# Kernel optimization log

Hardware: AMD Instinct MI355X
Metric: run time of the kernel (lower is better)

The kernel has to match this reference:

```python
import math
import jax, jax.numpy as jnp
import numpy as np

N = 50000       # num_nodes
D = 128         # input feature dim
OUT = 128       # output_dim
H = 8           # num_heads
F = OUT // H    # out_feats per head (= self_attn hidden_dim)
E_RAND = 800000 # random edges per graph (+ N self loops)
ALPHA = 0.8
BETA = 0.5


def _edges(key):
    k1, k2 = jax.random.split(key)
    src = jax.random.randint(k1, (E_RAND,), 0, N, dtype=jnp.int32)
    dst = jax.random.randint(k2, (E_RAND,), 0, N, dtype=jnp.int32)
    loop = jnp.arange(N, dtype=jnp.int32)  # dgl.add_self_loop
    return jnp.concatenate([src, loop]), jnp.concatenate([dst, loop])


def setup_inputs() -> dict:
    key = jax.random.key(0)
    ks = jax.random.split(key, 32)
    inp = {"x": jax.random.normal(ks[0], (N, D), jnp.float32)}
    inp["src_s"], inp["dst_s"] = _edges(ks[1])
    inp["src_t"], inp["dst_t"] = _edges(ks[2])
    inp["src_p"], inp["dst_p"] = _edges(ks[3])
    i = 4
    for v in ("s", "t", "p"):
        inp[f"W_{v}"] = jax.random.normal(ks[i], (OUT, D), jnp.float32) * 0.05; i += 1
        inp[f"al_{v}"] = jax.random.normal(ks[i], (H, F), jnp.float32) * 0.1; i += 1
        inp[f"ar_{v}"] = jax.random.normal(ks[i], (H, F), jnp.float32) * 0.1; i += 1
        inp[f"b_{v}"] = jnp.zeros((OUT,), jnp.float32)
    inp["Wq"] = jax.random.normal(ks[i], (F, OUT), jnp.float32) * 0.05; i += 1
    inp["bq"] = jnp.zeros((F,), jnp.float32)
    inp["Wk"] = jax.random.normal(ks[i], (F, OUT), jnp.float32) * 0.05; i += 1
    inp["bk"] = jnp.zeros((F,), jnp.float32)
    inp["Wm"] = jax.random.normal(ks[i], (1, N * OUT), jnp.float32) * 0.001; i += 1
    inp["bm"] = jnp.zeros((1,), jnp.float32)
    return inp


def _gat(x, src, dst, W, al, ar, b):
    # DGL GATConv (eval mode, negative_slope=0.2, activation=relu)
    feat = (x @ W.T).reshape(N, H, F)                      # [N,H,F]
    el = jnp.einsum('nhf,hf->nh', feat, al)                # [N,H]
    er = jnp.einsum('nhf,hf->nh', feat, ar)
    e = jax.nn.leaky_relu(el[src] + er[dst], 0.2)          # [E,H]
    m = jax.ops.segment_max(e, dst, num_segments=N)        # per-dst softmax
    ex = jnp.exp(e - m[dst])
    s = jax.ops.segment_sum(ex, dst, num_segments=N)
    attn = ex / s[dst]                                     # [E,H]
    out = jax.ops.segment_sum(feat[src] * attn[:, :, None], dst, num_segments=N)
    return jax.nn.relu(out + b.reshape(1, H, F)).reshape(N, OUT)


def reference(x, src_s, dst_s, src_t, dst_t, src_p, dst_p,
              W_s, al_s, ar_s, b_s, W_t, al_t, ar_t, b_t,
              W_p, al_p, ar_p, b_p, Wq, bq, Wk, bk, Wm, bm):
    s = _gat(x, src_s, dst_s, W_s, al_s, ar_s, b_s)
    t = _gat(x, src_t, dst_t, W_t, al_t, ar_t, b_t)
    p = _gat(x, src_p, dst_p, W_p, al_p, ar_p, b_p)
    views = jnp.stack([s, t, p])                           # [3,N,OUT]
    # self_attn: one scalar attention weight per view
    Q = jnp.einsum('vne,he->vnh', views, Wq) + bq          # [3,N,F]
    K = jnp.einsum('vne,he->vnh', views, Wk) + bk
    logits = jnp.sum(Q.reshape(3, -1) * K.reshape(3, -1), -1) / math.sqrt(F * N)
    w = jax.nn.softmax(logits)                             # [3]
    fused = w[:, None, None] * views
    views2 = ALPHA * fused + (1.0 - ALPHA) * views         # [3,N,OUT]
    # mv_attn: sigmoid-gated sum of views
    omega = jax.nn.sigmoid(views2.reshape(3, -1) @ Wm.T + bm)[:, 0]  # [3]
    mv = jnp.einsum('v,vne->ne', omega, views2)            # [N,OUT]
    result = BETA * views2 + (1.0 - BETA) * mv[None]       # [3,N,OUT]
    return mv, result
```

## Files before the change

### kernel.cpp

```cpp
#include <hip/hip_runtime.h>


#define N_NODES 50000
#define DIM 128
#define OUTD 128
#define NH 8
#define NF 16
#define NE 850000
#define NOFF 50001
#define NBUCK 49
#define BCAP 20480
#define BIN_EPT 8
#define BIN_EPB 2048

typedef float f32x4 __attribute__((ext_vector_type(4)));
typedef float f32x2 __attribute__((ext_vector_type(2)));
typedef __bf16 bf16x8 __attribute__((ext_vector_type(8)));
typedef unsigned short u16x8 __attribute__((ext_vector_type(8)));

static __device__ __forceinline__ float bf2f_lo(unsigned int u) {
  return __uint_as_float(u << 16);
}
static __device__ __forceinline__ float bf2f_hi(unsigned int u) {
  return __uint_as_float(u & 0xffff0000u);
}
static __device__ __forceinline__ f32x2 up2(unsigned int u) {
  f32x2 r;
  r.x = __uint_as_float(u << 16);
  r.y = __uint_as_float(u & 0xffff0000u);
  return r;
}
static __device__ __forceinline__ unsigned short f2bf(float f) {
  unsigned int u = __float_as_uint(f);
  unsigned int r = (u + 0x7fffu + ((u >> 16) & 1u)) >> 16;
  return (unsigned short)r;
}

__global__ __launch_bounds__(256) void gemm_feat_kernel(
    const float* __restrict__ x, const float* __restrict__ Ws,
    const float* __restrict__ Wt, const float* __restrict__ Wp,
    unsigned short* __restrict__ feat) {
  __shared__ unsigned short xa[128 * 128];
  __shared__ unsigned short wb[128 * 128];
  const int t = threadIdx.x;
  const int n0 = blockIdx.x * 128;

  for (int i = 0; i < 16; ++i) {
    int flat = (i * 256 + t) * 4;
    int r = flat >> 7, c = flat & 127;
    float4 val = make_float4(0.f, 0.f, 0.f, 0.f);
    if (n0 + r < N_NODES) val = *(const float4*)(x + (size_t)(n0 + r) * DIM + c);
    int byteoff = (r * 256 + c * 2) ^ ((r & 7) << 4);
    unsigned short* p = (unsigned short*)((char*)xa + byteoff);
    p[0] = f2bf(val.x); p[1] = f2bf(val.y); p[2] = f2bf(val.z); p[3] = f2bf(val.w);
  }

  const int wave = t >> 6, lane = t & 63;
  const int wr = wave >> 1, wc = wave & 1;
  const int lrow = lane & 15;
  const int kgrp = lane >> 4;

  for (int v = 0; v < 3; ++v) {
    const float* W = (v == 0) ? Ws : ((v == 1) ? Wt : Wp);
    __syncthreads();
    for (int i = 0; i < 16; ++i) {
      int flat = (i * 256 + t) * 4;
      int r = flat >> 7, c = flat & 127;
      float4 val = *(const float4*)(W + r * DIM + c);
      int byteoff = (r * 256 + c * 2) ^ ((r & 7) << 4);
      unsigned short* p = (unsigned short*)((char*)wb + byteoff);
      p[0] = f2bf(val.x); p[1] = f2bf(val.y); p[2] = f2bf(val.z); p[3] = f2bf(val.w);
    }
    __syncthreads();

    f32x4 acc[4][4];
    for (int m = 0; m < 4; ++m)
      for (int n = 0; n < 4; ++n) acc[m][n] = (f32x4)0.f;

    for (int ks = 0; ks < 4; ++ks) {
      bf16x8 af[4], bfr[4];
      int kb2 = (ks * 32 + kgrp * 8) * 2;
      for (int m = 0; m < 4; ++m) {
        int r = wr * 64 + m * 16 + lrow;
        af[m] = *(const bf16x8*)((const char*)xa + ((r * 256 + kb2) ^ ((r & 7) << 4)));
      }
      for (int n = 0; n < 4; ++n) {
        int r = wc * 64 + n * 16 + lrow;
        bfr[n] = *(const bf16x8*)((const char*)wb + ((r * 256 + kb2) ^ ((r & 7) << 4)));
      }
      for (int m = 0; m < 4; ++m)
        for (int n = 0; n < 4; ++n)
          acc[m][n] = __builtin_amdgcn_mfma_f32_16x16x32_bf16(af[m], bfr[n], acc[m][n], 0, 0, 0);
    }

    unsigned short* fv = feat + (size_t)v * N_NODES * OUTD;
    for (int m = 0; m < 4; ++m)
      for (int n = 0; n < 4; ++n) {
        int col = wc * 64 + n * 16 + lrow;
        for (int r4 = 0; r4 < 4; ++r4) {
          int row = n0 + wr * 64 + m * 16 + kgrp * 4 + r4;
          if (row < N_NODES) fv[(size_t)row * OUTD + col] = f2bf(acc[m][n][r4]);
        }
      }
  }
}

__global__ __launch_bounds__(256) void elr_kernel(
    const unsigned short* __restrict__ feat,
    const float* __restrict__ al_s, const float* __restrict__ ar_s,
    const float* __restrict__ al_t, const float* __restrict__ ar_t,
    const float* __restrict__ al_p, const float* __restrict__ ar_p,
    float* __restrict__ el, float* __restrict__ er) {
  int idx = blockIdx.x * 256 + threadIdx.x;
  if (idx >= 3 * N_NODES * NH) return;
  int v = idx / (N_NODES * NH);
  int rem = idx - v * (N_NODES * NH);
  int n = rem >> 3, h = rem & 7;
  const float* al = (v == 0) ? al_s : ((v == 1) ? al_t : al_p);
  const float* ar = (v == 0) ? ar_s : ((v == 1) ? ar_t : ar_p);
  const unsigned short* fr = feat + (size_t)v * N_NODES * OUTD + (size_t)n * OUTD + h * NF;
  uint4 a = *(const uint4*)(fr);
  uint4 b = *(const uint4*)(fr + 8);
  float fv[16];
  fv[0] = bf2f_lo(a.x); fv[1] = bf2f_hi(a.x); fv[2] = bf2f_lo(a.y); fv[3] = bf2f_hi(a.y);
  fv[4] = bf2f_lo(a.z); fv[5] = bf2f_hi(a.z); fv[6] = bf2f_lo(a.w); fv[7] = bf2f_hi(a.w);
  fv[8] = bf2f_lo(b.x); fv[9] = bf2f_hi(b.x); fv[10] = bf2f_lo(b.y); fv[11] = bf2f_hi(b.y);
  fv[12] = bf2f_lo(b.z); fv[13] = bf2f_hi(b.z); fv[14] = bf2f_lo(b.w); fv[15] = bf2f_hi(b.w);
  float accl = 0.f, accr = 0.f;
#pragma unroll
  for (int f = 0; f < NF; ++f) {
    accl += fv[f] * al[h * NF + f];
    accr += fv[f] * ar[h * NF + f];
  }
  el[idx] = accl;
  er[idx] = accr;
}

__global__ __launch_bounds__(256) void bin_kernel(
    const int* __restrict__ src_s, const int* __restrict__ dst_s,
    const int* __restrict__ src_t, const int* __restrict__ dst_t,
    const int* __restrict__ src_p, const int* __restrict__ dst_p,
    int* __restrict__ gtail, unsigned int* __restrict__ gbin) {
  const int v = blockIdx.y;
  const int* S = (v == 0) ? src_s : ((v == 1) ? src_t : src_p);
  const int* D = (v == 0) ? dst_s : ((v == 1) ? dst_t : dst_p);
  __shared__ int lhist[4][64], lbase[4][64];
  const int t = threadIdx.x;
  const int wave = t >> 6;
  ((int*)lhist)[t] = 0;
  __syncthreads();
  const int e0 = blockIdx.x * BIN_EPB + t * BIN_EPT;
  unsigned int pk[BIN_EPT];
  int bk[BIN_EPT], rk[BIN_EPT];
#pragma unroll
  for (int i = 0; i < BIN_EPT; ++i) {
    int e = e0 + i;
    if (e < NE) {
      unsigned int s = (unsigned int)S[e], d = (unsigned int)D[e];
      pk[i] = (s << 16) | d;
      bk[i] = (int)(d >> 10);
      rk[i] = atomicAdd(&lhist[wave][bk[i]], 1);
    } else {
      bk[i] = -1;
    }
  }
  __syncthreads();
  if (t < 64) {
    int c0 = lhist[0][t], c1 = lhist[1][t], c2 = lhist[2][t], c3 = lhist[3][t];
    int tot = c0 + c1 + c2 + c3;
    int gb = (tot > 0) ? atomicAdd(&gtail[v * 64 + t], tot) : 0;
    lbase[0][t] = gb;
    lbase[1][t] = gb + c0;
    lbase[2][t] = gb + c0 + c1;
    lbase[3][t] = gb + c0 + c1 + c2;
  }
  __syncthreads();
#pragma unroll
  for (int i = 0; i < BIN_EPT; ++i) {
    if (bk[i] >= 0) {
      int pos = lbase[wave][bk[i]] + rk[i];
      if (pos < BCAP)
        gbin[((size_t)v * 64 + bk[i]) * BCAP + pos] = pk[i];
    }
  }
}

__global__ __launch_bounds__(1024) void bucket_sort_kernel(
    const int* __restrict__ gtail, const unsigned int* __restrict__ gbin,
    int* __restrict__ offs, int* __restrict__ esrc) {
  __shared__ int lcur[1024];
  __shared__ int wsum[16];
  __shared__ int sh_bbase;
  __shared__ unsigned int sorted[BCAP];
  __shared__ int lhist[1024];
  const int v = blockIdx.y;
  const int b = blockIdx.x;
  const int t = threadIdx.x;
  const int wave = t >> 6, lane = t & 63;

  int cnt = gtail[v * 64 + b];
  if (cnt > BCAP) cnt = BCAP;
  const unsigned int* eb = gbin + ((size_t)v * 64 + b) * BCAP;

  if (t < 64) {
    int valb = (t < b) ? gtail[v * 64 + t] : 0;
#pragma unroll
    for (int m = 1; m < 64; m <<= 1) valb += __shfl_xor(valb, m, 64);
    if (t == 0) sh_bbase = valb;
  }
  lhist[t] = 0;
  __syncthreads();

  for (int e = t; e < cnt; e += 1024)
    atomicAdd(&lhist[eb[e] & 1023u], 1);
  __syncthreads();

  int val = lhist[t];
  int incl = val;
#pragma unroll
  for (int st = 1; st < 64; st <<= 1) {
    int o = __shfl_up(incl, st, 64);
    if (lane >= st) incl += o;
  }
  if (lane == 63) wsum[wave] = incl;
  __syncthreads();
  if (t < 64) {
    int wv = (lane < 16) ? wsum[lane] : 0;
    int winc = wv;
#pragma unroll
    for (int st = 1; st < 16; st <<= 1) {
      int o = __shfl_up(winc, st, 64);
      if (lane >= st) winc += o;
    }
    if (lane < 16) wsum[lane] = winc - wv;
  }
  __syncthreads();
  const int base = wsum[wave] + incl - val;
  lcur[t] = base;

  const int bbase = sh_bbase;
  if (b == 0 && t == 0) offs[v * NOFF] = 0;
  {
    int n = b * 1024 + t;
    if (n < N_NODES) offs[v * NOFF + n + 1] = bbase + base + val;
  }
  __syncthreads();

  for (int e = t; e < cnt; e += 1024) {
    unsigned int pk = eb[e];
    int pos = atomicAdd(&lcur[pk & 1023u], 1);
    sorted[pos] = pk >> 16;
  }
  __syncthreads();

  int* ev = esrc + (size_t)v * NE + bbase;
  for (int e = t; e < cnt; e += 1024) ev[e] = (int)sorted[e];
}

__global__ __launch_bounds__(256) void gat_kernel(
    const int* __restrict__ offs, const int* __restrict__ esrc,
    const float* __restrict__ el, const float* __restrict__ er,
    const unsigned short* __restrict__ feat,
    const float* __restrict__ b_s, const float* __restrict__ b_t,
    const float* __restrict__ b_p, float* __restrict__ views) {
  const int v = blockIdx.y;
  const int n = blockIdx.x * 4 + (threadIdx.x >> 6);
  const int lane = threadIdx.x & 63;
  const int g = lane >> 4;
  const int q = lane & 15;
  const int h = q >> 1;
  const int* off_v = offs + v * NOFF;
  const int off0 = off_v[n];
  const int deg = off_v[n + 1] - off0;
  const int* es = esrc + (size_t)v * NE + off0;
  const float* el_v = el + (size_t)v * N_NODES * NH;
  const float er_h = er[((size_t)v * N_NODES + n) * NH + h];
  const unsigned short* featv = feat + (size_t)v * N_NODES * OUTD;

  f32x2 acc2[4];
#pragma unroll
  for (int j = 0; j < 4; ++j) acc2[j] = (f32x2)0.f;
  float sm = 0.f;

  int e0 = g, e1 = 4 + g;
  bool v0 = e0 < deg, v1 = e1 < deg;
  int s0 = es[v0 ? e0 : 0];
  int s1 = es[v1 ? e1 : 0];
  float l0 = el_v[s0 * NH + h];
  float l1 = el_v[s1 * NH + h];
  uint4 pk0 = *(const uint4*)(featv + (size_t)s0 * OUTD + q * 8);
  uint4 pk1 = *(const uint4*)(featv + (size_t)s1 * OUTD + q * 8);

  for (int base = 0; base < deg; base += 8) {
    bool cv0 = v0, cv1 = v1;
    float cl0 = l0, cl1 = l1;
    uint4 cp0 = pk0, cp1 = pk1;
    int nb = base + 8;
    if (nb < deg) {
      e0 = nb + g; e1 = nb + 4 + g;
      v0 = e0 < deg; v1 = e1 < deg;
      s0 = es[v0 ? e0 : 0];
      s1 = es[v1 ? e1 : 0];
      l0 = el_v[s0 * NH + h];
      l1 = el_v[s1 * NH + h];
      pk0 = *(const uint4*)(featv + (size_t)s0 * OUTD + q * 8);
      pk1 = *(const uint4*)(featv + (size_t)s1 * OUTD + q * 8);
    }
    float val0 = cl0 + er_h;
    float val1 = cl1 + er_h;
    val0 = fmaxf(val0, 0.2f * val0);
    val1 = fmaxf(val1, 0.2f * val1);
    float aw0 = cv0 ? __expf(val0) : 0.f;
    float aw1 = cv1 ? __expf(val1) : 0.f;
    sm += aw0 + aw1;
    acc2[0] += aw0 * up2(cp0.x) + aw1 * up2(cp1.x);
    acc2[1] += aw0 * up2(cp0.y) + aw1 * up2(cp1.y);
    acc2[2] += aw0 * up2(cp0.z) + aw1 * up2(cp1.z);
    acc2[3] += aw0 * up2(cp0.w) + aw1 * up2(cp1.w);
  }

#pragma unroll
  for (int m = 16; m < 64; m <<= 1) {
    sm += __shfl_xor(sm, m, 64);
#pragma unroll
    for (int j = 0; j < 4; ++j) {
      acc2[j].x += __shfl_xor(acc2[j].x, m, 64);
      acc2[j].y += __shfl_xor(acc2[j].y, m, 64);
    }
  }

  if (g == 0) {
    const float inv = 1.0f / sm;
    const float* bv = (v == 0) ? b_s : ((v == 1) ? b_t : b_p);
    float r[8];
#pragma unroll
    for (int j = 0; j < 4; ++j) {
      float x0 = acc2[j].x * inv + bv[q * 8 + 2 * j];
      float x1 = acc2[j].y * inv + bv[q * 8 + 2 * j + 1];
      r[2 * j] = (x0 > 0.f) ? x0 : 0.f;
      r[2 * j + 1] = (x1 > 0.f) ? x1 : 0.f;
    }
    float* dst = views + (size_t)v * N_NODES * OUTD + (size_t)n * OUTD + q * 8;
    *(float4*)(dst) = make_float4(r[0], r[1], r[2], r[3]);
    *(float4*)(dst + 4) = make_float4(r[4], r[5], r[6], r[7]);
  }
}

__global__ __launch_bounds__(256) void viewred_kernel(
    const float* __restrict__ views, const float* __restrict__ Wq,
    const float* __restrict__ bq, const float* __restrict__ Wk,
    const float* __restrict__ bk, const float* __restrict__ Wm,
    float* __restrict__ logits, float* __restrict__ dsum) {
  __shared__ unsigned short vt[128 * 128];
  __shared__ unsigned short wq[16 * 128];
  __shared__ unsigned short wk[16 * 128];
  __shared__ float redq[4], redd[4];
  const int n0 = blockIdx.x * 128;
  const int t = threadIdx.x;
  const int wave = t >> 6, lane = t & 63;
  const int lrow = lane & 15;
  const int kgrp = lane >> 4;

  {
    int flat = t * 8;
    int r = flat >> 7, c = flat & 127;
    int byteoff = (r * 256 + c * 2) ^ ((r & 7) << 4);
    float4 qa = *(const float4*)(Wq + flat);
    float4 qb = *(const float4*)(Wq + flat + 4);
    u16x8 oq;
    oq[0] = f2bf(qa.x); oq[1] = f2bf(qa.y); oq[2] = f2bf(qa.z); oq[3] = f2bf(qa.w);
    oq[4] = f2bf(qb.x); oq[5] = f2bf(qb.y); oq[6] = f2bf(qb.z); oq[7] = f2bf(qb.w);
    *(u16x8*)((char*)wq + byteoff) = oq;
    float4 ka = *(const float4*)(Wk + flat);
    float4 kb = *(const float4*)(Wk + flat + 4);
    u16x8 ok;
    ok[0] = f2bf(ka.x); ok[1] = f2bf(ka.y); ok[2] = f2bf(ka.z); ok[3] = f2bf(ka.w);
    ok[4] = f2bf(kb.x); ok[5] = f2bf(kb.y); ok[6] = f2bf(kb.z); ok[7] = f2bf(kb.w);
    *(u16x8*)((char*)wk + byteoff) = ok;
  }

  const float bqv = bq[lrow];
  const float bkv = bk[lrow];

  for (int v = 0; v < 3; ++v) {
    const float* Vv = views + (size_t)v * N_NODES * OUTD;
    float dp = 0.f;
    for (int i = 0; i < 8; ++i) {
      int flat = (i * 256 + t) * 8;
      int r = flat >> 7, c = flat & 127;
      int row = n0 + r;
      u16x8 o = (u16x8)0;
      if (row < N_NODES) {
        size_t goff = (size_t)row * OUTD + c;
        float4 a = *(const float4*)(Vv + goff);
        float4 b = *(const float4*)(Vv + goff + 4);
        float4 wa = *(const float4*)(Wm + goff);
        float4 wb2 = *(const float4*)(Wm + goff + 4);
        dp += a.x * wa.x + a.y * wa.y + a.z * wa.z + a.w * wa.w;
        dp += b.x * wb2.x + b.y * wb2.y + b.z * wb2.z + b.w * wb2.w;
        o[0] = f2bf(a.x); o[1] = f2bf(a.y); o[2] = f2bf(a.z); o[3] = f2bf(a.w);
        o[4] = f2bf(b.x); o[5] = f2bf(b.y); o[6] = f2bf(b.z); o[7] = f2bf(b.w);
      }
      int byteoff = (r * 256 + c * 2) ^ ((r & 7) << 4);
      *(u16x8*)((char*)vt + byteoff) = o;
    }
    __syncthreads();

    float qk = 0.f;
    f32x4 accQ[2], accK[2];
    accQ[0] = (f32x4)0.f; accQ[1] = (f32x4)0.f;
    accK[0] = (f32x4)0.f; accK[1] = (f32x4)0.f;
    for (int ks = 0; ks < 4; ++ks) {
      int kb2 = (ks * 32 + kgrp * 8) * 2;
      int rb = lrow;
      bf16x8 bqf = *(const bf16x8*)((const char*)wq + ((rb * 256 + kb2) ^ ((rb & 7) << 4)));
      bf16x8 bkf = *(const bf16x8*)((const char*)wk + ((rb * 256 + kb2) ^ ((rb & 7) << 4)));
#pragma unroll
      for (int m = 0; m < 2; ++m) {
        int r = (wave * 2 + m) * 16 + lrow;
        bf16x8 af = *(const bf16x8*)((const char*)vt + ((r * 256 + kb2) ^ ((r & 7) << 4)));
        accQ[m] = __builtin_amdgcn_mfma_f32_16x16x32_bf16(af, bqf, accQ[m], 0, 0, 0);
        accK[m] = __builtin_amdgcn_mfma_f32_16x16x32_bf16(af, bkf, accK[m], 0, 0, 0);
      }
    }
#pragma unroll
    for (int m = 0; m < 2; ++m) {
#pragma unroll
      for (int j = 0; j < 4; ++j) {
        int row = n0 + (wave * 2 + m) * 16 + kgrp * 4 + j;
        if (row < N_NODES) qk += (accQ[m][j] + bqv) * (accK[m][j] + bkv);
      }
    }

#pragma unroll
    for (int m = 1; m < 64; m <<= 1) {
      qk += __shfl_xor(qk, m, 64);
      dp += __shfl_xor(dp, m, 64);
    }
    if (lane == 0) { redq[wave] = qk; redd[wave] = dp; }
    __syncthreads();
    if (t == 0) {
      atomicAdd(&logits[v], redq[0] + redq[1] + redq[2] + redq[3]);
      atomicAdd(&dsum[v], redd[0] + redd[1] + redd[2] + redd[3]);
    }
    __syncthreads();
  }
}

__global__ void scalar_kernel(const float* __restrict__ logits,
                              const float* __restrict__ dsum,
                              const float* __restrict__ bm, float* __restrict__ gc) {
  if (threadIdx.x == 0 && blockIdx.x == 0) {
    const float scale = 1.0f / sqrtf((float)(NF * N_NODES));
    float l0 = logits[0] * scale, l1 = logits[1] * scale, l2 = logits[2] * scale;
    float mx = fmaxf(l0, fmaxf(l1, l2));
    float e0 = __expf(l0 - mx), e1 = __expf(l1 - mx), e2 = __expf(l2 - mx);
    float inv = 1.0f / (e0 + e1 + e2);
    float g0 = 0.8f * e0 * inv + 0.2f;
    float g1 = 0.8f * e1 * inv + 0.2f;
    float g2 = 0.8f * e2 * inv + 0.2f;
    float bmv = bm[0];
    float o0 = 1.0f / (1.0f + __expf(-(g0 * dsum[0] + bmv)));
    float o1 = 1.0f / (1.0f + __expf(-(g1 * dsum[1] + bmv)));
    float o2 = 1.0f / (1.0f + __expf(-(g2 * dsum[2] + bmv)));
    gc[0] = g0; gc[1] = g1; gc[2] = g2;
    gc[3] = o0 * g0; gc[4] = o1 * g1; gc[5] = o2 * g2;
  }
}

__global__ __launch_bounds__(256) void final_kernel(
    const float* __restrict__ views, const float* __restrict__ gc,
    float* __restrict__ out) {
  const size_t NT = (size_t)N_NODES * OUTD;
  size_t base = ((size_t)blockIdx.x * 256 + threadIdx.x) * 4;
  if (base >= NT) return;
  float g0 = gc[0], g1 = gc[1], g2 = gc[2], c0 = gc[3], c1 = gc[4], c2 = gc[5];
  float4 a0 = *(const float4*)(views + base);
  float4 a1 = *(const float4*)(views + NT + base);
  float4 a2 = *(const float4*)(views + 2 * NT + base);
  float4 mv;
  mv.x = c0 * a0.x + c1 * a1.x + c2 * a2.x;
  mv.y = c0 * a0.y + c1 * a1.y + c2 * a2.y;
  mv.z = c0 * a0.z + c1 * a1.z + c2 * a2.z;
  mv.w = c0 * a0.w + c1 * a1.w + c2 * a2.w;
  *(float4*)(out + base) = mv;
  float4 r;
  r.x = 0.5f * (g0 * a0.x) + 0.5f * mv.x;
  r.y = 0.5f * (g0 * a0.y) + 0.5f * mv.y;
  r.z = 0.5f * (g0 * a0.z) + 0.5f * mv.z;
  r.w = 0.5f * (g0 * a0.w) + 0.5f * mv.w;
  *(float4*)(out + NT + base) = r;
  r.x = 0.5f * (g1 * a1.x) + 0.5f * mv.x;
  r.y = 0.5f * (g1 * a1.y) + 0.5f * mv.y;
  r.z = 0.5f * (g1 * a1.z) + 0.5f * mv.z;
  r.w = 0.5f * (g1 * a1.w) + 0.5f * mv.w;
  *(float4*)(out + 2 * NT + base) = r;
  r.x = 0.5f * (g2 * a2.x) + 0.5f * mv.x;
  r.y = 0.5f * (g2 * a2.y) + 0.5f * mv.y;
  r.z = 0.5f * (g2 * a2.z) + 0.5f * mv.z;
  r.w = 0.5f * (g2 * a2.w) + 0.5f * mv.w;
  *(float4*)(out + 3 * NT + base) = r;
}

extern "C" void kernel_launch(void* const* d_in, const int* in_sizes, int n_in,
                              void* d_out, int out_size, void* d_ws, size_t ws_size,
                              hipStream_t stream) {
  const float* x = (const float*)d_in[0];
  const int* src_s = (const int*)d_in[1];
  const int* dst_s = (const int*)d_in[2];
  const int* src_t = (const int*)d_in[3];
  const int* dst_t = (const int*)d_in[4];
  const int* src_p = (const int*)d_in[5];
  const int* dst_p = (const int*)d_in[6];
  const float* W_s = (const float*)d_in[7];
  const float* al_s = (const float*)d_in[8];
  const float* ar_s = (const float*)d_in[9];
  const float* b_s = (const float*)d_in[10];
  const float* W_t = (const float*)d_in[11];
  const float* al_t = (const float*)d_in[12];
  const float* ar_t = (const float*)d_in[13];
  const float* b_t = (const float*)d_in[14];
  const float* W_p = (const float*)d_in[15];
  const float* al_p = (const float*)d_in[16];
  const float* ar_p = (const float*)d_in[17];
  const float* b_p = (const float*)d_in[18];
  const float* Wq = (const float*)d_in[19];
  const float* bq = (const float*)d_in[20];
  const float* Wk = (const float*)d_in[21];
  const float* bk = (const float*)d_in[22];
  const float* Wm = (const float*)d_in[23];
  const float* bm = (const float*)d_in[24];
  float* out = (float*)d_out;

  char* ws = (char*)d_ws;
  unsigned short* feat = (unsigned short*)ws;
  float* el = (float*)(ws + 38400000);
  float* er = (float*)(ws + 43200000);
  float* views = (float*)(ws + 48000000);
  int* offs = (int*)(ws + 124800000);
  int* esrc = (int*)(ws + 126000016);
  int* gtail = (int*)(ws + 136800016);
  float* scal = (float*)(ws + 136800784);

  unsigned int* gbin = (unsigned int*)(ws + 49000000);

  hipMemsetAsync(gtail, 0, 768 + 48, stream);

  gemm_feat_kernel<<<dim3(391), dim3(256), 0, stream>>>(x, W_s, W_t, W_p, feat);
  elr_kernel<<<dim3((3 * N_NODES * NH + 255) / 256), dim3(256), 0, stream>>>(
      feat, al_s, ar_s, al_t, ar_t, al_p, ar_p, el, er);
  bin_kernel<<<dim3((NE + BIN_EPB - 1) / BIN_EPB, 3), dim3(256), 0, stream>>>(
      src_s, dst_s, src_t, dst_t, src_p, dst_p, gtail, gbin);
  bucket_sort_kernel<<<dim3(NBUCK, 3), dim3(1024), 0, stream>>>(
      gtail, gbin, offs, esrc);
  gat_kernel<<<dim3(12500, 3), dim3(256), 0, stream>>>(
      offs, esrc, el, er, feat, b_s, b_t, b_p, views);
  viewred_kernel<<<dim3(391), dim3(256), 0, stream>>>(
      views, Wq, bq, Wk, bk, Wm, scal, scal + 3);
  scalar_kernel<<<dim3(1), dim3(64), 0, stream>>>(scal, scal + 3, bm, scal + 6);
  final_kernel<<<dim3(6250), dim3(256), 0, stream>>>(views, scal + 6, out);
}
```

Measured before the change: 418.9 us.

## Fuse el/er projection into GEMM epilogue and remap GAT lanes per edge

The GEMM kernel now stages each bf16 output tile in shared memory, writes feat with vectorized coalesced stores, and computes the per-head el/er dot products in the same pass. This removes the separate elr kernel and its re-read of feat. The GAT aggregation kernel also changes lane mapping so that 8 lanes cover one edge (one head each, 16 features) and 8 edges are processed per iteration instead of 4 edges x 2. That gives one exp per lane and wider loads, at the cost of more accumulator registers and a longer shuffle reduction.

```diff
diff --git a/kernel.cpp b/kernel.cpp
--- a/kernel.cpp
+++ b/kernel.cpp
@@ -39,9 +39,14 @@
 __global__ __launch_bounds__(256) void gemm_feat_kernel(
     const float* __restrict__ x, const float* __restrict__ Ws,
     const float* __restrict__ Wt, const float* __restrict__ Wp,
-    unsigned short* __restrict__ feat) {
+    const float* __restrict__ al_s, const float* __restrict__ ar_s,
+    const float* __restrict__ al_t, const float* __restrict__ ar_t,
+    const float* __restrict__ al_p, const float* __restrict__ ar_p,
+    unsigned short* __restrict__ feat, float* __restrict__ el,
+    float* __restrict__ er) {
   __shared__ unsigned short xa[128 * 128];
   __shared__ unsigned short wb[128 * 128];
+  __shared__ float alS[128], arS[128];
   const int t = threadIdx.x;
   const int n0 = blockIdx.x * 128;
 
@@ -59,9 +64,13 @@
   const int wr = wave >> 1, wc = wave & 1;
   const int lrow = lane & 15;
   const int kgrp = lane >> 4;
+  const int row = t >> 1, half = t & 1;
+  const int grow = n0 + row;
 
   for (int v = 0; v < 3; ++v) {
     const float* W = (v == 0) ? Ws : ((v == 1) ? Wt : Wp);
+    const float* alv = (v == 0) ? al_s : ((v == 1) ? al_t : al_p);
+    const float* arv = (v == 0) ? ar_s : ((v == 1) ? ar_t : ar_p);
     __syncthreads();
     for (int i = 0; i < 16; ++i) {
       int flat = (i * 256 + t) * 4;
@@ -71,6 +80,8 @@
       unsigned short* p = (unsigned short*)((char*)wb + byteoff);
       p[0] = f2bf(val.x); p[1] = f2bf(val.y); p[2] = f2bf(val.z); p[3] = f2bf(val.w);
     }
+    if (t < 128) alS[t] = alv[t];
+    else arS[t - 128] = arv[t - 128];
     __syncthreads();
 
     f32x4 acc[4][4];
@@ -93,47 +104,52 @@
           acc[m][n] = __builtin_amdgcn_mfma_f32_16x16x32_bf16(af[m], bfr[n], acc[m][n], 0, 0, 0);
     }
 
-    unsigned short* fv = feat + (size_t)v * N_NODES * OUTD;
+    __syncthreads();
     for (int m = 0; m < 4; ++m)
       for (int n = 0; n < 4; ++n) {
         int col = wc * 64 + n * 16 + lrow;
+#pragma unroll
         for (int r4 = 0; r4 < 4; ++r4) {
-          int row = n0 + wr * 64 + m * 16 + kgrp * 4 + r4;
-          if (row < N_NODES) fv[(size_t)row * OUTD + col] = f2bf(acc[m][n][r4]);
+          int r = wr * 64 + m * 16 + kgrp * 4 + r4;
+          int bo = (r * 256 + col * 2) ^ ((r & 7) << 4);
+          *(unsigned short*)((char*)wb + bo) = f2bf(acc[m][n][r4]);
         }
       }
-  }
-}
-
-__global__ __launch_bounds__(256) void elr_kernel(
-    const unsigned short* __restrict__ feat,
-    const float* __restrict__ al_s, const float* __restrict__ ar_s,
-    const float* __restrict__ al_t, const float* __restrict__ ar_t,
-    const float* __restrict__ al_p, const float* __restrict__ ar_p,
-    float* __restrict__ el, float* __restrict__ er) {
-  int idx = blockIdx.x * 256 + threadIdx.x;
-  if (idx >= 3 * N_NODES * NH) return;
-  int v = idx / (N_NODES * NH);
-  int rem = idx - v * (N_NODES * NH);
-  int n = rem >> 3, h = rem & 7;
-  const float* al = (v == 0) ? al_s : ((v == 1) ? al_t : al_p);
-  const float* ar = (v == 0) ? ar_s : ((v == 1) ? ar_t : ar_p);
-  const unsigned short* fr = feat + (size_t)v * N_NODES * OUTD + (size_t)n * OUTD + h * NF;
-  uint4 a = *(const uint4*)(fr);
-  uint4 b = *(const uint4*)(fr + 8);
-  float fv[16];
-  fv[0] = bf2f_lo(a.x); fv[1] = bf2f_hi(a.x); fv[2] = bf2f_lo(a.y); fv[3] = bf2f_hi(a.y);
-  fv[4] = bf2f_lo(a.z); fv[5] = bf2f_hi(a.z); fv[6] = bf2f_lo(a.w); fv[7] = bf2f_hi(a.w);
-  fv[8] = bf2f_lo(b.x); fv[9] = bf2f_hi(b.x); fv[10] = bf2f_lo(b.y); fv[11] = bf2f_hi(b.y);
-  fv[12] = bf2f_lo(b.z); fv[13] = bf2f_hi(b.z); fv[14] = bf2f_lo(b.w); fv[15] = bf2f_hi(b.w);
-  float accl = 0.f, accr = 0.f;
-#pragma unroll
-  for (int f = 0; f < NF; ++f) {
-    accl += fv[f] * al[h * NF + f];
-    accr += fv[f] * ar[h * NF + f];
-  }
-  el[idx] = accl;
-  er[idx] = accr;
+    __syncthreads();
+
+    unsigned short* fv = feat + (size_t)v * N_NODES * OUTD;
+    if (grow < N_NODES) {
+      const int cb = half * 64;
+#pragma unroll
+      for (int i = 0; i < 8; ++i) {
+        int c = cb + i * 8;
+        u16x8 val = *(const u16x8*)((const char*)wb + ((row * 256 + c * 2) ^ ((row & 7) << 4)));
+        *(u16x8*)(fv + (size_t)grow * OUTD + c) = val;
+      }
+      float4 elq, erq;
+      float* elp = (float*)&elq;
+      float* erp = (float*)&erq;
+#pragma unroll
+      for (int k = 0; k < 4; ++k) {
+        int h = half * 4 + k;
+        int c = h * 16;
+        u16x8 f0 = *(const u16x8*)((const char*)wb + ((row * 256 + c * 2) ^ ((row & 7) << 4)));
+        u16x8 f1 = *(const u16x8*)((const char*)wb + ((row * 256 + (c + 8) * 2) ^ ((row & 7) << 4)));
+        float accl = 0.f, accr = 0.f;
+#pragma unroll
+        for (int f = 0; f < 8; ++f) {
+          float v0 = bf2f_lo((unsigned int)(unsigned short)f0[f]);
+          float v1 = bf2f_lo((unsigned int)(unsigned short)f1[f]);
+          accl += v0 * alS[c + f] + v1 * alS[c + 8 + f];
+          accr += v0 * arS[c + f] + v1 * arS[c + 8 + f];
+        }
+        elp[k] = accl; erp[k] = accr;
+      }
+      size_t eo = ((size_t)v * N_NODES + n0) * NH + t * 4;
+      *(float4*)(el + eo) = elq;
+      *(float4*)(er + eo) = erq;
+    }
+  }
 }
 
 __global__ __launch_bounds__(256) void bin_kernel(
@@ -266,83 +282,78 @@
   const int v = blockIdx.y;
   const int n = blockIdx.x * 4 + (threadIdx.x >> 6);
   const int lane = threadIdx.x & 63;
-  const int g = lane >> 4;
-  const int q = lane & 15;
-  const int h = q >> 1;
+  const int g = lane >> 3;
+  const int q = lane & 7;
   const int* off_v = offs + v * NOFF;
   const int off0 = off_v[n];
   const int deg = off_v[n + 1] - off0;
   const int* es = esrc + (size_t)v * NE + off0;
   const float* el_v = el + (size_t)v * N_NODES * NH;
-  const float er_h = er[((size_t)v * N_NODES + n) * NH + h];
+  const float er_q = er[((size_t)v * N_NODES + n) * NH + q];
   const unsigned short* featv = feat + (size_t)v * N_NODES * OUTD;
 
-  f32x2 acc2[4];
-#pragma unroll
-  for (int j = 0; j < 4; ++j) acc2[j] = (f32x2)0.f;
+  f32x2 acc[8];
+#pragma unroll
+  for (int j = 0; j < 8; ++j) acc[j] = (f32x2)0.f;
   float sm = 0.f;
 
-  int e0 = g, e1 = 4 + g;
-  bool v0 = e0 < deg, v1 = e1 < deg;
-  int s0 = es[v0 ? e0 : 0];
-  int s1 = es[v1 ? e1 : 0];
-  float l0 = el_v[s0 * NH + h];
-  float l1 = el_v[s1 * NH + h];
-  uint4 pk0 = *(const uint4*)(featv + (size_t)s0 * OUTD + q * 8);
-  uint4 pk1 = *(const uint4*)(featv + (size_t)s1 * OUTD + q * 8);
+  int e = g;
+  bool vld = e < deg;
+  int s = es[vld ? e : 0];
+  float l = el_v[s * NH + q];
+  const unsigned short* fp = featv + (size_t)s * OUTD + q * 16;
+  uint4 a0 = *(const uint4*)(fp);
+  uint4 a1 = *(const uint4*)(fp + 8);
 
   for (int base = 0; base < deg; base += 8) {
-    bool cv0 = v0, cv1 = v1;
-    float cl0 = l0, cl1 = l1;
-    uint4 cp0 = pk0, cp1 = pk1;
+    bool cvld = vld;
+    float cl = l;
+    uint4 c0 = a0, c1 = a1;
     int nb = base + 8;
     if (nb < deg) {
-      e0 = nb + g; e1 = nb + 4 + g;
-      v0 = e0 < deg; v1 = e1 < deg;
-      s0 = es[v0 ? e0 : 0];
-      s1 = es[v1 ? e1 : 0];
-      l0 = el_v[s0 * NH + h];
-      l1 = el_v[s1 * NH + h];
-      pk0 = *(const uint4*)(featv + (size_t)s0 * OUTD + q * 8);
-      pk1 = *(const uint4*)(featv + (size_t)s1 * OUTD + q * 8);
-    }
-    float val0 = cl0 + er_h;
-    float val1 = cl1 + er_h;
-    val0 = fmaxf(val0, 0.2f * val0);
-    val1 = fmaxf(val1, 0.2f * val1);
-    float aw0 = cv0 ? __expf(val0) : 0.f;
-    float aw1 = cv1 ? __expf(val1) : 0.f;
-    sm += aw0 + aw1;
-    acc2[0] += aw0 * up2(cp0.x) + aw1 * up2(cp1.x);
-    acc2[1] += aw0 * up2(cp0.y) + aw1 * up2(cp1.y);
-    acc2[2] += aw0 * up2(cp0.z) + aw1 * up2(cp1.z);
-    acc2[3] += aw0 * up2(cp0.w) + aw1 * up2(cp1.w);
-  }
-
-#pragma unroll
-  for (int m = 16; m < 64; m <<= 1) {
+      e = nb + g;
+      vld = e < deg;
+      s = es[vld ? e : 0];
+      l = el_v[s * NH + q];
+      fp = featv + (size_t)s * OUTD + q * 16;
+      a0 = *(const uint4*)(fp);
+      a1 = *(const uint4*)(fp + 8);
+    }
+    float val = cl + er_q;
+    val = fmaxf(val, 0.2f * val);
+    float aw = cvld ? __expf(val) : 0.f;
+    sm += aw;
+    acc[0] += aw * up2(c0.x);
+    acc[1] += aw * up2(c0.y);
+    acc[2] += aw * up2(c0.z);
+    acc[3] += aw * up2(c0.w);
+    acc[4] += aw * up2(c1.x);
+    acc[5] += aw * up2(c1.y);
+    acc[6] += aw * up2(c1.z);
+    acc[7] += aw * up2(c1.w);
+  }
+
+#pragma unroll
+  for (int m = 8; m < 64; m <<= 1) {
     sm += __shfl_xor(sm, m, 64);
 #pragma unroll
-    for (int j = 0; j < 4; ++j) {
-      acc2[j].x += __shfl_xor(acc2[j].x, m, 64);
-      acc2[j].y += __shfl_xor(acc2[j].y, m, 64);
-    }
-  }
-
-  if (g == 0) {
+    for (int j = 0; j < 8; ++j) {
+      acc[j].x += __shfl_xor(acc[j].x, m, 64);
+      acc[j].y += __shfl_xor(acc[j].y, m, 64);
+    }
+  }
+
+  if (g < 4) {
     const float inv = 1.0f / sm;
     const float* bv = (v == 0) ? b_s : ((v == 1) ? b_t : b_p);
-    float r[8];
-#pragma unroll
-    for (int j = 0; j < 4; ++j) {
-      float x0 = acc2[j].x * inv + bv[q * 8 + 2 * j];
-      float x1 = acc2[j].y * inv + bv[q * 8 + 2 * j + 1];
-      r[2 * j] = (x0 > 0.f) ? x0 : 0.f;
-      r[2 * j + 1] = (x1 > 0.f) ? x1 : 0.f;
-    }
-    float* dst = views + (size_t)v * N_NODES * OUTD + (size_t)n * OUTD + q * 8;
-    *(float4*)(dst) = make_float4(r[0], r[1], r[2], r[3]);
-    *(float4*)(dst + 4) = make_float4(r[4], r[5], r[6], r[7]);
+    int f0 = q * 16 + g * 4;
+    float x0 = acc[2 * g].x * inv + bv[f0 + 0];
+    float x1 = acc[2 * g].y * inv + bv[f0 + 1];
+    float x2 = acc[2 * g + 1].x * inv + bv[f0 + 2];
+    float x3 = acc[2 * g + 1].y * inv + bv[f0 + 3];
+    float4 r = make_float4(fmaxf(x0, 0.f), fmaxf(x1, 0.f), fmaxf(x2, 0.f),
+                           fmaxf(x3, 0.f));
+    *(float4*)(views + ((size_t)v * N_NODES + n) * OUTD + f0) = r;
   }
 }
 
@@ -546,9 +557,8 @@
 
   hipMemsetAsync(gtail, 0, 768 + 48, stream);
 
-  gemm_feat_kernel<<<dim3(391), dim3(256), 0, stream>>>(x, W_s, W_t, W_p, feat);
-  elr_kernel<<<dim3((3 * N_NODES * NH + 255) / 256), dim3(256), 0, stream>>>(
-      feat, al_s, ar_s, al_t, ar_t, al_p, ar_p, el, er);
+  gemm_feat_kernel<<<dim3(391), dim3(256), 0, stream>>>(
+      x, W_s, W_t, W_p, al_s, ar_s, al_t, ar_t, al_p, ar_p, feat, el, er);
   bin_kernel<<<dim3((NE + BIN_EPB - 1) / BIN_EPB, 3), dim3(256), 0, stream>>>(
       src_s, dst_s, src_t, dst_t, src_p, dst_p, gtail, gbin);
   bucket_sort_kernel<<<dim3(NBUCK, 3), dim3(1024), 0, stream>>>(
```

Result: slower. 441.4 us (+5.4%).
